# Performance work log

Hardware: AMD Instinct MI355X
Metric: run time of the kernel (lower is better)

The kernel has to match this reference:

```python
import jax, jax.numpy as jnp
import numpy as np

K = 75        # kpoints
L = 8         # number of labels (output_dim)


def _knn_nonconformity(q, t, train_label, k=K, num_labels=L):
    """Brute-force kNN (Euclidean) + distance-weighted nonconformity.
    q: [B, D] queries; t: [N, D] train bank; train_label: [N] int.
    Returns [B, num_labels]: for each class i, sum of 1/dist over the k
    nearest neighbors whose label != i (0 weight for zero distance)."""
    # squared distances [B, N]
    d2 = (jnp.sum(q * q, axis=1, keepdims=True)
          - 2.0 * q @ t.T
          + jnp.sum(t * t, axis=1)[None, :])
    d2 = jnp.maximum(d2, 0.0)
    neg_top, idx = jax.lax.top_k(-d2, k)          # k smallest d2
    dist = jnp.sqrt(jnp.maximum(-neg_top, 0.0))    # [B, k]
    safe = jnp.where(dist > 0, dist, 1.0)
    w = jnp.where(dist > 0, 1.0 / safe, 0.0)       # [B, k]
    mismatch = 1.0 - jax.nn.one_hot(train_label[idx], num_labels, dtype=w.dtype)  # [B,k,L]
    return jnp.einsum('bk,bkl->bl', w, mismatch)


def setup_inputs() -> dict:
    key = jax.random.key(0)
    ks = jax.random.split(key, 12)
    B, N, D, H, C = 1024, 50000, 83, 128, 10000
    s = lambda fan_in: 1.0 / np.sqrt(fan_in)
    return {
        'x': jax.random.normal(ks[0], (B, D), jnp.float32),
        'train_x': jax.random.normal(ks[1], (N, D), jnp.float32),
        'train_label': jax.random.randint(ks[2], (N,), 0, L, jnp.int32),
        'cali': jax.random.uniform(ks[3], (C,), jnp.float32) * 50.0,
        'W1': jax.random.normal(ks[4], (D, H), jnp.float32) * s(D),
        'b1': jnp.zeros((H,), jnp.float32),
        'W2': jax.random.normal(ks[5], (H, H), jnp.float32) * s(H),
        'b2': jnp.zeros((H,), jnp.float32),
        'W3': jax.random.normal(ks[6], (H, H), jnp.float32) * s(H),
        'b3': jnp.zeros((H,), jnp.float32),
        'W4': jax.random.normal(ks[7], (H, L), jnp.float32) * s(H),
        'b4': jnp.zeros((L,), jnp.float32),
    }


def reference(x, train_x, train_label, cali, W1, b1, W2, b2, W3, b3, W4, b4):
    relu = jax.nn.relu
    # query-side MLP (inference: dropout inactive)
    h1 = relu(x @ W1 + b1)
    h2 = relu(h1 @ W2 + b2)
    h3 = relu(h2 @ W3 + b3)
    out = jax.nn.softmax(h3 @ W4 + b4, axis=-1)
    # train-side feature banks (what each kNTree was fit on)
    t1 = relu(train_x @ W1 + b1)
    t2 = relu(t1 @ W2 + b2)
    t3 = relu(t2 @ W3 + b3)
    t4 = jax.nn.softmax(t3 @ W4 + b4, axis=-1)
    # per-layer nonconformity [B, L], summed across the 5 layers
    total = (_knn_nonconformity(x, train_x, train_label)
             + _knn_nonconformity(h1, t1, train_label)
             + _knn_nonconformity(h2, t2, train_label)
             + _knn_nonconformity(h3, t3, train_label)
             + _knn_nonconformity(out, t4, train_label))
    # empirical p-value: fraction of calibration scores >= total nonconformity
    counts = jnp.sum(cali[None, None, :] >= total[:, :, None], axis=-1)  # [B, L]
    return counts.astype(jnp.float32) / cali.shape[0]
```

## Files before the change

kernel.cpp:

```cpp
#include <hip/hip_runtime.h>
#include <math.h>

#define KNN 75
#define NL 8
#define NB 1024
#define NT 50000
#define NT_PAD 50048
#define NCALI 10000
#define KC 32
#define TT 128
#define NTB 391
#define SLOTS 16
#define CAP 6144
#define NSUB 2048
#define NSB 16
#define SSTRIDE 24
#define SOFF 11
#define RSEL 32
#define MLP8_BQ 1563
#define MLPB (2*NTB+16)
#define ARENA 34816

#define PB_Q    384
#define PB_BANK 18750
#define PB_W1   48
#define PB_W23  64
#define PREP_BLOCKS (PB_Q+PB_BANK+PB_W1+2*PB_W23)

typedef __attribute__((ext_vector_type(8))) short bf16x8;
typedef __attribute__((ext_vector_type(4))) float f32x4;

__device__ __forceinline__ int swz(int c){ return c + ((c>>5)<<2); }

__device__ __forceinline__ unsigned short f2bf_rn(float x){
  unsigned u = __float_as_uint(x);
  unsigned r = (u + 0x7FFFu + ((u>>16)&1u)) >> 16;
  return (unsigned short)r;
}
__device__ __forceinline__ float bf2f(unsigned short h){
  return __uint_as_float(((unsigned)h)<<16);
}
__device__ __forceinline__ bf16x8 ld8(const unsigned short* p){
  return *(const bf16x8*)p;
}
__device__ __forceinline__ void gl_lds16(const unsigned short* g, unsigned short* l){
  __builtin_amdgcn_global_load_lds(
      (const __attribute__((address_space(1))) void*)g,
      (__attribute__((address_space(3))) void*)l, 16, 0, 0);
}

__device__ __forceinline__ void pad_one(const float* __restrict__ in,
                                        float* __restrict__ out, int M,
                                        int Din, int Dout, int idx){
  if (idx >= M*Dout) return;
  int r = idx / Dout, c = idx - r*Dout;
  out[idx] = (c < Din) ? in[r*Din + c] : 0.f;
}
__device__ __forceinline__ void wsplit_one(const float* __restrict__ W, int kreal,
                                           int dp, unsigned short* __restrict__ WtH,
                                           unsigned short* __restrict__ WtL, int idx){
  int n = idx / dp, k = idx - n*dp;
  float v = (k < kreal) ? W[(size_t)k*128 + n] : 0.f;
  unsigned short h = f2bf_rn(v);
  WtH[idx] = h;
  WtL[idx] = f2bf_rn(v - bf2f(h));
}
__global__ void prep_k(const float* __restrict__ x, float* __restrict__ xq0,
                       const float* __restrict__ txr, float* __restrict__ tbA,
                       const float* __restrict__ W1, unsigned short* wt1H, unsigned short* wt1L,
                       const float* __restrict__ W2, unsigned short* wt2H, unsigned short* wt2L,
                       const float* __restrict__ W3, unsigned short* wt3H, unsigned short* wt3L){
  int b = blockIdx.x, tid = threadIdx.x;
  if (b < PB_Q){
    pad_one(x, xq0, NB, 83, 96, b*256 + tid);
  } else if (b < PB_Q + PB_BANK){
    pad_one(txr, tbA, NT, 83, 96, (b-PB_Q)*256 + tid);
  } else if (b < PB_Q + PB_BANK + PB_W1){
    wsplit_one(W1, 83, 96,  wt1H, wt1L, (b-PB_Q-PB_BANK)*256 + tid);
  } else if (b < PB_Q + PB_BANK + PB_W1 + PB_W23){
    wsplit_one(W2, 128, 128, wt2H, wt2L, (b-PB_Q-PB_BANK-PB_W1)*256 + tid);
  } else {
    wsplit_one(W3, 128, 128, wt3H, wt3L, (b-PB_Q-PB_BANK-PB_W1-PB_W23)*256 + tid);
  }
}

__global__ void conv_norm_k(
    const float* __restrict__ XA, unsigned short* __restrict__ HA,
    unsigned short* __restrict__ LA, float* __restrict__ nA, int MA,
    const float* __restrict__ XB, unsigned short* __restrict__ HB,
    unsigned short* __restrict__ LB, float* __restrict__ nB, int MB,
    int dp)
{
  int w = threadIdx.x>>6, lane = threadIdx.x&63;
  int row = blockIdx.x*4 + w;
  const float* src; unsigned short* dh; unsigned short* dl; float* nrm;
  if (row < MA){
    src=&XA[(size_t)row*dp]; dh=&HA[(size_t)row*dp]; dl=&LA[(size_t)row*dp]; nrm=&nA[row];
  } else {
    int r2 = row - MA;
    if (r2 >= MB) return;
    src=&XB[(size_t)r2*dp]; dh=&HB[(size_t)r2*dp]; dl=&LB[(size_t)r2*dp]; nrm=&nB[r2];
  }
  float s=0.f;
  for (int c=lane*2; c<dp; c+=128){
    float2 v = *(const float2*)&src[c];
    s += v.x*v.x + v.y*v.y;
    unsigned short h0 = f2bf_rn(v.x), h1 = f2bf_rn(v.y);
    float r0 = v.x - bf2f(h0), r1 = v.y - bf2f(h1);
    ushort2 hh; hh.x=h0; hh.y=h1;
    ushort2 ll; ll.x=f2bf_rn(r0); ll.y=f2bf_rn(r1);
    *(ushort2*)&dh[c]=hh;
    *(ushort2*)&dl[c]=ll;
  }
  #pragma unroll
  for (int off=32;off>0;off>>=1) s += __shfl_down(s, off, 64);
  if (lane==0) *nrm=s;
}

__device__ __forceinline__ void find_bin(int* hist, int* part, int nb, int Krem,
                                         int tid, int* s_B, int* s_lob){
  int ch = nb>>8;
  int base = tid*ch;
  int s=0;
  for (int b=base;b<base+ch;b++) s+=hist[b];
  int lane = tid & 63, wv = tid>>6;
  int v = s;
  #pragma unroll
  for (int off=1; off<64; off<<=1){
    int u = __shfl_up(v, off, 64);
    if (lane >= off) v += u;
  }
  if (lane==63) part[wv] = v;
  __syncthreads();
  int wbase = 0;
  #pragma unroll
  for (int w2=0; w2<4; w2++) wbase += (w2 < wv) ? part[w2] : 0;
  v += wbase;
  int excl = v - s;
  if (v >= Krem && excl < Krem){
    int lob = excl, B = base + ch - 1;
    for (int b=base;b<base+ch;b++){
      if (lob + hist[b] >= Krem){ B=b; break; }
      lob += hist[b];
    }
    *s_B = B; *s_lob = lob;
  }
  if (tid==255 && v < Krem){ *s_B = nb-1; *s_lob = 0; }
  __syncthreads();
}

__global__ __launch_bounds__(256) void sel64_k(const unsigned* __restrict__ skeys,
                                               unsigned* __restrict__ Tthr){
  __shared__ unsigned buf[NSUB];
  __shared__ int hist[2048];
  __shared__ int part[256];
  __shared__ int sB, sLob;
  int tid=threadIdx.x, q=blockIdx.x;
  for (int i=tid;i<NSUB;i+=256) buf[i]=skeys[(size_t)q*NSUB+i];
  int Krem=RSEL;
  for (int i=tid;i<2048;i+=256) hist[i]=0;
  __syncthreads();
  for (int i=tid;i<NSUB;i+=256) atomicAdd(&hist[buf[i]>>21],1);
  __syncthreads();
  find_bin(hist,part,2048,Krem,tid,&sB,&sLob);
  unsigned pre=(unsigned)sB; Krem-=sLob;
  for (int i=tid;i<2048;i+=256) hist[i]=0;
  __syncthreads();
  for (int i=tid;i<NSUB;i+=256){ unsigned k=buf[i]; if ((k>>21)==pre) atomicAdd(&hist[(k>>10)&0x7FFu],1); }
  __syncthreads();
  find_bin(hist,part,2048,Krem,tid,&sB,&sLob);
  pre=(pre<<11)|(unsigned)sB; Krem-=sLob;
  for (int i=tid;i<1024;i+=256) hist[i]=0;
  __syncthreads();
  for (int i=tid;i<NSUB;i+=256){ unsigned k=buf[i]; if ((k>>10)==pre) atomicAdd(&hist[k&0x3FFu],1); }
  __syncthreads();
  find_bin(hist,part,1024,Krem,tid,&sB,&sLob);
  if (tid==0) Tthr[q]=(pre<<10)|(unsigned)sB;
}

#define MFMA_SEC(BHC, BLC, AH, AL)                                               \
  _Pragma("unroll")                                                              \
  for (int tj=0;tj<8;tj++){                                                      \
    int rowB = tj*16 + col;                                                      \
    int sw = (((quad + (rowB>>1)) & 3) << 3);                                    \
    bf16x8 bh = *(const bf16x8*)&(BHC)[rowB*32 + sw];                            \
    bf16x8 bl = *(const bf16x8*)&(BLC)[rowB*32 + sw];                            \
    acc[tj] = __builtin_amdgcn_mfma_f32_16x16x32_bf16(AH, bh, acc[tj], 0,0,0);   \
    acc[tj] = __builtin_amdgcn_mfma_f32_16x16x32_bf16(AH, bl, acc[tj], 0,0,0);   \
    acc[tj] = __builtin_amdgcn_mfma_f32_16x16x32_bf16(AL, bh, acc[tj], 0,0,0);   \
  }

#define MFMA_KLOOP(ROWMAP)                                                       \
  size_t aoff = (size_t)(qbase + w*16 + col)*dp + quad*8;                        \
  const unsigned short* pAH = QH + aoff;                                         \
  const unsigned short* pAL = QL + aoff;                                         \
  int i0 = tid,      row0 = i0>>2, sg0 = ((i0&3) - (row0>>1)) & 3;               \
  int i1 = tid+256,  row1 = i1>>2, sg1 = ((i1&3) - (row1>>1)) & 3;               \
  size_t g0 = (size_t)(ROWMAP(n0+row0))*dp + (size_t)sg0*8;                      \
  size_t g1 = (size_t)(ROWMAP(n0+row1))*dp + (size_t)sg1*8;                      \
  f32x4 acc[8];                                                                  \
  _Pragma("unroll")                                                              \
  for (int tj=0;tj<8;tj++){ f32x4 z={0.f,0.f,0.f,0.f}; acc[tj]=z; }              \
  gl_lds16(TH + g0, BH0 + i0*8);                                                 \
  gl_lds16(TH + g1, BH0 + i1*8);                                                 \
  gl_lds16(TL + g0, BL0 + i0*8);                                                 \
  gl_lds16(TL + g1, BL0 + i1*8);                                                 \
  bf16x8 xh = ld8(pAH), xl = ld8(pAL);                                           \
  bf16x8 yh = xh, yl = xl;                                                       \
  _Pragma("unroll")                                                              \
  for (int kc=0; kc<kchunks; kc+=2){                                             \
    __syncthreads();                                                             \
    if (kc+1 < kchunks){                                                         \
      size_t ko=(size_t)(kc+1)*32;                                               \
      gl_lds16(TH + g0 + ko, BH1 + i0*8);                                        \
      gl_lds16(TH + g1 + ko, BH1 + i1*8);                                        \
      gl_lds16(TL + g0 + ko, BL1 + i0*8);                                        \
      gl_lds16(TL + g1 + ko, BL1 + i1*8);                                        \
      yh = ld8(pAH + ko); yl = ld8(pAL + ko);                                    \
    }                                                                            \
    MFMA_SEC(BH0, BL0, xh, xl);                                                  \
    if (kc+1 < kchunks){                                                         \
      __syncthreads();                                                           \
      if (kc+2 < kchunks){                                                       \
        size_t ko=(size_t)(kc+2)*32;                                             \
        gl_lds16(TH + g0 + ko, BH0 + i0*8);                                      \
        gl_lds16(TH + g1 + ko, BH0 + i1*8);                                      \
        gl_lds16(TL + g0 + ko, BL0 + i0*8);                                      \
        gl_lds16(TL + g1 + ko, BL0 + i1*8);                                      \
        xh = ld8(pAH + ko); xl = ld8(pAL + ko);                                  \
      }                                                                          \
      MFMA_SEC(BH1, BL1, yh, yl);                                                \
    }                                                                            \
  }

#define ROW_ID(r) (r)
#define ROW_SUB(r) ((r)*SSTRIDE + SOFF)

template<int KCH>
__global__ __launch_bounds__(256) void dist_mfma_k(
    const unsigned short* __restrict__ QH, const unsigned short* __restrict__ QL,
    const unsigned short* __restrict__ TH, const unsigned short* __restrict__ TL,
    const float* __restrict__ qn, const float* __restrict__ tn,
    const int* __restrict__ labels, const unsigned* __restrict__ Tthr,
    unsigned* __restrict__ slab)
{
  constexpr int dp = KCH*32;
  __shared__ __align__(16) unsigned short smem[4*4096];
  unsigned short* BH0 = smem;
  unsigned short* BH1 = smem + 4096;
  unsigned short* BL0 = smem + 8192;
  unsigned short* BL1 = smem + 12288;
  unsigned (*hitbuf)[SLOTS] = (unsigned (*)[SLOTS])smem;
  int* hcnt = (int*)(smem + 4096);
  int b = blockIdx.x;
  int xcd = b & 7, s = b >> 3;
  int qb = s & 15, tslot = s >> 4;
  int t_blk = xcd + 8*tslot;
  if (t_blk >= NTB) return;
  int tid = threadIdx.x, w = tid>>6, lane = tid&63;
  int quad = lane>>4, col = lane&15;
  int qbase = qb*64;
  int n0 = t_blk*TT;
  constexpr int kchunks = KCH;

  MFMA_KLOOP(ROW_ID)

  __syncthreads();
  if (tid<64) hcnt[tid]=0;
  __syncthreads();
  float qnr[4]; unsigned Tq[4]; float thrF[4];
  #pragma unroll
  for (int r=0;r<4;r++){
    int q = qbase + w*16 + quad*4 + r;
    qnr[r]  = qn[q];
    Tq[r]   = Tthr[q];
    thrF[r] = __uint_as_float(Tq[r] | 7u);
  }
  #pragma unroll
  for (int tj=0;tj<8;tj++){
    int t = n0 + tj*16 + col;
    if (t < NT){
      float tnv = tn[t];
      unsigned lab = (unsigned)labels[t];
      #pragma unroll
      for (int r=0;r<4;r++){
        float d2 = fmaf(-2.f, acc[tj][r], qnr[r] + tnv);
        if (d2 <= thrF[r]){
          float d2c = fmaxf(d2, 0.f);
          unsigned key = (__float_as_uint(d2c)&0xFFFFFFF8u) | lab;
          if (key < Tq[r]){
            int ql = w*16 + quad*4 + r;
            int idx = atomicAdd(&hcnt[ql], 1);
            if (idx < SLOTS-1) hitbuf[ql][1+idx] = key;
          }
        }
      }
    }
  }
  __syncthreads();
  if (tid<64) hitbuf[tid][0]=(unsigned)hcnt[tid];
  __syncthreads();
  {
    int q = tid>>2, sub = (tid&3)*4;
    uint4 v = *(uint4*)&hitbuf[q][sub];
    *(uint4*)&slab[((size_t)(qbase+q)*NTB + t_blk)*SLOTS + sub] = v;
  }
}

template<int KCH>
__device__ __forceinline__ void distsub_body(char* smc, int b,
    const unsigned short* __restrict__ QH, const unsigned short* __restrict__ QL,
    const unsigned short* __restrict__ TH, const unsigned short* __restrict__ TL,
    const float* __restrict__ qn, const float* __restrict__ tn,
    const int* __restrict__ labels, unsigned* __restrict__ keys)
{
  constexpr int dp = KCH*32;
  unsigned short* BH0 = (unsigned short*)smc;
  unsigned short* BH1 = BH0 + 4096;
  unsigned short* BL0 = BH0 + 8192;
  unsigned short* BL1 = BH0 + 12288;
  int qb = b & 15, t_blk = b >> 4;
  int tid = threadIdx.x, w = tid>>6, lane = tid&63;
  int quad = lane>>4, col = lane&15;
  int qbase = qb*64;
  int n0 = t_blk*TT;
  constexpr int kchunks = KCH;

  MFMA_KLOOP(ROW_SUB)

  float qnr[4];
  #pragma unroll
  for (int r=0;r<4;r++)
    qnr[r] = qn[qbase + w*16 + quad*4 + r];
  #pragma unroll
  for (int tj=0;tj<8;tj++){
    int sI = n0 + tj*16 + col;
    int g  = sI*SSTRIDE + SOFF;
    float tnv = tn[g];
    unsigned lab = (unsigned)labels[g];
    #pragma unroll
    for (int r=0;r<4;r++){
      float d2 = fmaxf(fmaf(-2.f, acc[tj][r], qnr[r] + tnv), 0.f);
      unsigned key = (__float_as_uint(d2)&0xFFFFFFF8u) | lab;
      int q = qbase + w*16 + quad*4 + r;
      keys[(size_t)q*NSUB + sI] = key;
    }
  }
}

template<int KCH>
__device__ __forceinline__ void mlp_body(char* smc, int b,
    const unsigned short* __restrict__ bkH, const unsigned short* __restrict__ bkL,
    const unsigned short* __restrict__ qh,  const unsigned short* __restrict__ ql,
    const unsigned short* __restrict__ TH, const unsigned short* __restrict__ TL,
    const float* __restrict__ bias,
    float* __restrict__ OutB, unsigned short* __restrict__ SBH,
    unsigned short* __restrict__ SBL, float* __restrict__ nrmB,
    float* __restrict__ OutQ, unsigned short* __restrict__ SQH,
    unsigned short* __restrict__ SQL, float* __restrict__ nrmQ)
{
  constexpr int dp = KCH*32;
  unsigned short* BH0 = (unsigned short*)smc;
  unsigned short* BH1 = BH0 + 4096;
  unsigned short* BL0 = BH0 + 8192;
  unsigned short* BL1 = BH0 + 12288;
  bool isq = (b >= 2*NTB);
  const unsigned short* QH = isq ? qh : bkH;
  const unsigned short* QL = isq ? ql : bkL;
  float* Out = isq ? OutQ : OutB;
  unsigned short* SH = isq ? SQH : SBH;
  unsigned short* SL = isq ? SQL : SBL;
  float* nrm = isq ? nrmQ : nrmB;
  int M = isq ? NB : NT;
  int tid = threadIdx.x, w = tid>>6, lane = tid&63;
  int quad = lane>>4, col = lane&15;
  int qbase = (isq ? (b - 2*NTB) : b) * 64;
  int n0 = 0;
  constexpr int kchunks = KCH;

  MFMA_KLOOP(ROW_ID)

  float bb[8];
  #pragma unroll
  for (int tj=0;tj<8;tj++) bb[tj] = bias[tj*16 + col];
  #pragma unroll
  for (int r=0;r<4;r++){
    int row = qbase + w*16 + quad*4 + r;
    if (row < M){
      float vv[8]; float s=0.f;
      #pragma unroll
      for (int tj=0;tj<8;tj++){
        float v = acc[tj][r] + bb[tj];
        v = v > 0.f ? v : 0.f;
        vv[tj] = v;
        s += v*v;
        Out[(size_t)row*128 + tj*16 + col] = v;
      }
      #pragma unroll
      for (int off=1; off<16; off<<=1) s += __shfl_xor(s, off, 16);
      if (col==0) nrm[row] = s;
      #pragma unroll
      for (int tj=0;tj<8;tj++){
        unsigned short h = f2bf_rn(vv[tj]);
        SH[(size_t)row*128 + tj*16 + col] = h;
        SL[(size_t)row*128 + tj*16 + col] = f2bf_rn(vv[tj] - bf2f(h));
      }
    }
  }
}

template<int KCH>
__global__ __launch_bounds__(256) void mlp_mfma_k(
    const unsigned short* bkH, const unsigned short* bkL,
    const unsigned short* qh,  const unsigned short* ql,
    const unsigned short* TH, const unsigned short* TL,
    const float* bias,
    float* OutB, unsigned short* SBH, unsigned short* SBL, float* nrmB,
    float* OutQ, unsigned short* SQH, unsigned short* SQL, float* nrmQ)
{
  __shared__ __align__(16) char smc[32768];
  mlp_body<KCH>(smc, blockIdx.x, bkH,bkL,qh,ql,TH,TL,bias,
                OutB,SBH,SBL,nrmB,OutQ,SQH,SQL,nrmQ);
}

__device__ __forceinline__ void mlp8_body(char* smc, int b,
    const float* __restrict__ AB, const float* __restrict__ AQ,
    const float* __restrict__ W4, const float* __restrict__ b4,
    float* __restrict__ OutB, unsigned short* __restrict__ SBH,
    unsigned short* __restrict__ SBL, float* __restrict__ nrmB,
    float* __restrict__ OutQ, unsigned short* __restrict__ SQH,
    unsigned short* __restrict__ SQL, float* __restrict__ nrmQ)
{
  float* Ws = (float*)smc;
  int tid = threadIdx.x;
  for (int i=tid;i<1024;i+=256) Ws[i]=W4[i];
  __syncthreads();
  bool isq = (b >= MLP8_BQ);
  int r = (isq ? (b-MLP8_BQ) : b)*32 + (tid>>3), c = tid&7;
  int M = isq ? NB : NT;
  if (r >= M) return;
  const float* A = isq ? AQ : AB;
  float* Out = isq ? OutQ : OutB;
  unsigned short* SH = isq ? SQH : SBH;
  unsigned short* SL = isq ? SQL : SBL;
  float* nrm = isq ? nrmQ : nrmB;
  const float* a = &A[(size_t)r*128];
  float acc = b4[c];
  #pragma unroll 16
  for (int k=0;k<128;k++) acc += a[k]*Ws[k*8+c];
  int lane = tid & 63, base = lane & ~7;
  float v[8];
  #pragma unroll
  for (int j=0;j<8;j++) v[j] = __shfl(acc, base+j, 64);
  float m=-1e30f;
  #pragma unroll
  for (int j=0;j<8;j++) m = v[j]>m ? v[j] : m;
  float s=0.f;
  #pragma unroll
  for (int j=0;j<8;j++){ v[j]=__expf(v[j]-m); s+=v[j]; }
  float inv=1.f/s;
  float nn=0.f;
  #pragma unroll
  for (int j=0;j<8;j++){ float pv=v[j]*inv; v[j]=pv; nn+=pv*pv; }
  float* p = &Out[(size_t)r*32];
  float pv = v[c];
  p[c]    = pv;
  p[8+c]  = 0.f;
  p[16+c] = 0.f;
  p[24+c] = 0.f;
  unsigned short h = f2bf_rn(pv);
  SH[(size_t)r*32 + c]    = h;
  SL[(size_t)r*32 + c]    = f2bf_rn(pv - bf2f(h));
  SH[(size_t)r*32 + 8+c]  = 0; SL[(size_t)r*32 + 8+c]  = 0;
  SH[(size_t)r*32 + 16+c] = 0; SL[(size_t)r*32 + 16+c] = 0;
  SH[(size_t)r*32 + 24+c] = 0; SL[(size_t)r*32 + 24+c] = 0;
  if (c==0) nrm[r] = nn;
}

__device__ void final_body(char* sm, int q,
    const unsigned* __restrict__ slab,
    const float* __restrict__ Qm, const float* __restrict__ Tm,
    const float* __restrict__ qn, const float* __restrict__ tn,
    const int* __restrict__ labels,
    float* __restrict__ tot, int first, int dp)
{
  int* hist = (int*)sm;
  int* part = (int*)(sm+8192);
  unsigned* buf = (unsigned*)(sm+9216);
  unsigned* lowbuf = (unsigned*)(sm+33792);
  float* qrow = (float*)(sm+34176);
  int* s_i = (int*)(sm+34688);
  float* s_w = (float*)(sm+34708);
  int tid=threadIdx.x;
  if (tid==0){ for (int j=0;j<9;j++) s_w[j]=0.f; s_i[2]=0; s_i[3]=0; s_i[4]=0; }
  __syncthreads();

  const unsigned* sq = slab + (size_t)q*NTB*SLOTS;
  for (int sidx=tid; sidx<NTB; sidx+=256){
    const unsigned* s = sq + (size_t)sidx*SLOTS;
    uint4 a = *(const uint4*)s;
    unsigned cnt = a.x;
    if (cnt > SLOTS-1){ s_i[4]=1; continue; }
    if (!cnt) continue;
    int base = atomicAdd(&s_i[2], (int)cnt);
    if (base + (int)cnt <= CAP){
      buf[base] = a.y;
      if (cnt>=2) buf[base+1] = a.z;
      if (cnt>=3) buf[base+2] = a.w;
      for (unsigned w=4; w<=cnt; w++) buf[base+w-1] = s[w];
    }
  }
  __syncthreads();
  int total = s_i[2];
  int bad = s_i[4];

#define CONTRIB(kk) do{ float d2_=__uint_as_float((kk)&0xFFFFFFF8u); \
    if (d2_>0.f){ float w_=1.0f/sqrtf(d2_); \
      atomicAdd(&s_w[8],w_); atomicAdd(&s_w[(kk)&7u],w_); } }while(0)

  unsigned T; int Krem=KNN;
  if (!bad && total>=KNN && total<=CAP){
    for (int i=tid;i<2048;i+=256) hist[i]=0;
    __syncthreads();
    for (int i=tid;i<total;i+=256) atomicAdd(&hist[buf[i]>>21],1);
    __syncthreads();
    find_bin(hist,part,2048,Krem,tid,&s_i[0],&s_i[1]);
    unsigned pre=(unsigned)s_i[0]; Krem-=s_i[1];
    for (int i=tid;i<2048;i+=256) hist[i]=0;
    __syncthreads();
    for (int i=tid;i<total;i+=256){ unsigned k=buf[i]; if ((k>>21)==pre) atomicAdd(&hist[(k>>10)&0x7FFu],1); }
    __syncthreads();
    find_bin(hist,part,2048,Krem,tid,&s_i[0],&s_i[1]);
    pre=(pre<<11)|(unsigned)s_i[0]; Krem-=s_i[1];
    for (int i=tid;i<1024;i+=256) hist[i]=0;
    __syncthreads();
    for (int i=tid;i<total;i+=256){ unsigned k=buf[i]; if ((k>>10)==pre) atomicAdd(&hist[k&0x3FFu],1); }
    __syncthreads();
    find_bin(hist,part,1024,Krem,tid,&s_i[0],&s_i[1]);
    T=(pre<<10)|(unsigned)s_i[0]; Krem-=s_i[1];
    __syncthreads();
    for (int i=tid;i<total;i+=256){ unsigned k=buf[i]; if (k<T) CONTRIB(k); }
  } else {
    if (tid==0) s_i[2]=0;
    for (int i=tid;i<dp;i+=256) qrow[i]=Qm[(size_t)q*dp+i];
    __syncthreads();
    float qq=qn[q];
    auto KEY=[&](int t)->unsigned{
      const float* br=&Tm[(size_t)t*dp];
      float dot=0.f;
      for (int k2=0;k2<dp;k2++) dot+=qrow[k2]*br[k2];
      float d2=fmaxf(qq-2.f*dot+tn[t],0.f);
      return (__float_as_uint(d2)&0xFFFFFFF8u)|(unsigned)labels[t];
    };
    for (int i=tid;i<2048;i+=256) hist[i]=0;
    __syncthreads();
    for (int t=tid;t<NT;t+=256) atomicAdd(&hist[KEY(t)>>21],1);
    __syncthreads();
    find_bin(hist,part,2048,Krem,tid,&s_i[0],&s_i[1]);
    int c=hist[s_i[0]]; Krem-=s_i[1];
    unsigned prefix=(unsigned)s_i[0]; int shift=21;
    if (c > CAP){
      __syncthreads();
      for (int i=tid;i<2048;i+=256) hist[i]=0;
      __syncthreads();
      for (int t=tid;t<NT;t+=256){ unsigned k=KEY(t); if ((k>>21)==prefix) atomicAdd(&hist[(k>>10)&0x7FFu],1); }
      __syncthreads();
      find_bin(hist,part,2048,Krem,tid,&s_i[0],&s_i[1]);
      c=hist[s_i[0]]; Krem-=s_i[1]; prefix=(prefix<<11)|(unsigned)s_i[0]; shift=10;
    }
    if (c > CAP){
      __syncthreads();
      for (int i=tid;i<1024;i+=256) hist[i]=0;
      __syncthreads();
      for (int t=tid;t<NT;t+=256){ unsigned k=KEY(t); if ((k>>10)==prefix) atomicAdd(&hist[k&0x3FFu],1); }
      __syncthreads();
      find_bin(hist,part,1024,Krem,tid,&s_i[0],&s_i[1]);
      c=hist[s_i[0]]; Krem-=s_i[1]; prefix=(prefix<<10)|(unsigned)s_i[0]; shift=0;
    }
    if (c <= CAP){
      for (int t=tid;t<NT;t+=256){
        unsigned k=KEY(t); unsigned pp=k>>shift;
        if (pp==prefix){ int j=atomicAdd(&s_i[2],1); if (j<CAP) buf[j]=k; }
        else if (pp<prefix){ int j=atomicAdd(&s_i[3],1); if (j<96) lowbuf[j]=k; }
      }
      __syncthreads();
      int sh=shift;
      while (sh>0){
        int nsh=(sh==21)?10:0;
        int nb=1<<(sh-nsh);
        __syncthreads();
        for (int i=tid;i<nb;i+=256) hist[i]=0;
        __syncthreads();
        int cc=s_i[2];
        for (int i=tid;i<cc;i+=256) atomicAdd(&hist[(buf[i]>>nsh)&(unsigned)(nb-1)],1);
        __syncthreads();
        find_bin(hist,part,nb,Krem,tid,&s_i[0],&s_i[1]);
        Krem-=s_i[1]; prefix=(prefix<<(sh-nsh))|(unsigned)s_i[0]; sh=nsh;
      }
      T=prefix;
      __syncthreads();
      int lowc=s_i[3], cc=s_i[2];
      for (int i=tid;i<lowc;i+=256){ unsigned k=lowbuf[i]; CONTRIB(k); }
      for (int i=tid;i<cc;i+=256){ unsigned k=buf[i]; if (k<T) CONTRIB(k); }
    } else {
      T=prefix;
      for (int t=tid;t<NT;t+=256){ unsigned k=KEY(t); if (k<T) CONTRIB(k); }
    }
  }
  __syncthreads();
  if (tid==0){
    float d2=__uint_as_float(T&0xFFFFFFF8u);
    float w=(d2>0.f)?(1.0f/sqrtf(d2)):0.f;
    s_w[8] += (float)Krem*w;
    s_w[T&7u] += (float)Krem*w;
  }
  __syncthreads();
  if (tid<8){
    float contrib = s_w[8]-s_w[tid];
    size_t o=(size_t)q*NL+tid;
    tot[o] = first ? contrib : tot[o]+contrib;
  }
#undef CONTRIB
}

__global__ __launch_bounds__(256) void final_k(
    const unsigned* slab, const float* Qm, const float* Tm,
    const float* qn, const float* tn, const int* labels,
    float* tot, int first, int dp)
{
  __shared__ __align__(16) char sm[ARENA];
  final_body(sm, blockIdx.x, slab, Qm, Tm, qn, tn, labels, tot, first, dp);
}

template<int KSUB, int KMLP, int M8>
__global__ __launch_bounds__(256) void fused_k(
    int nf,
    const unsigned* slab, const float* Qm, const float* Tm,
    const float* qnF, const float* tnF, float* tot, int first, int dpF,
    const unsigned short* qhS, const unsigned short* qlS,
    const unsigned short* bkHS, const unsigned short* bkLS,
    const float* qnS, const float* tnS, unsigned* skeys,
    const int* labels,
    const unsigned short* bkHM, const unsigned short* bkLM,
    const unsigned short* qhM, const unsigned short* qlM,
    const unsigned short* wtH, const unsigned short* wtL, const float* bias,
    float* OutB, unsigned short* SBH, unsigned short* SBL, float* nrmB,
    float* OutQ, unsigned short* SQH, unsigned short* SQL, float* nrmQ,
    const float* AB8, const float* AQ8, const float* W4, const float* b4)
{
  __shared__ __align__(16) char sm[ARENA];
  int b = blockIdx.x;
  if (b < nf){
    final_body(sm, b, slab, Qm, Tm, qnF, tnF, labels, tot, first, dpF);
    return;
  }
  b -= nf;
  if (b < 16*NSB){
    distsub_body<KSUB>(sm, b, qhS, qlS, bkHS, bkLS, qnS, tnS, labels, skeys);
    return;
  }
  b -= 16*NSB;
  if constexpr (KMLP > 0){
    mlp_body<KMLP>(sm, b, bkHM,bkLM,qhM,qlM, wtH,wtL, bias,
                   OutB,SBH,SBL,nrmB,OutQ,SQH,SQL,nrmQ);
  } else if constexpr (M8){
    mlp8_body(sm, b, AB8, AQ8, W4, b4, OutB,SBH,SBL,nrmB,OutQ,SQH,SQL,nrmQ);
  }
}

__global__ void pvalue_k(const float* __restrict__ tot, const float* __restrict__ cali,
                         float* __restrict__ out){
  __shared__ float t8[NL];
  __shared__ int part[4][NL];
  int tid=threadIdx.x, q=blockIdx.x;
  if (tid<NL) t8[tid]=tot[(size_t)q*NL+tid];
  __syncthreads();
  float th[NL];
  #pragma unroll
  for (int c=0;c<NL;c++) th[c]=t8[c];
  int cnt[NL];
  #pragma unroll
  for (int c=0;c<NL;c++) cnt[c]=0;
  for (int i=tid;i<NCALI;i+=256){
    float v=cali[i];
    #pragma unroll
    for (int c=0;c<NL;c++) cnt[c] += (v>=th[c]) ? 1 : 0;
  }
  #pragma unroll
  for (int c=0;c<NL;c++){
    #pragma unroll
    for (int off=32;off>0;off>>=1) cnt[c]+=__shfl_down(cnt[c],off,64);
  }
  if ((tid&63)==0){
    #pragma unroll
    for (int c=0;c<NL;c++) part[tid>>6][c]=cnt[c];
  }
  __syncthreads();
  if (tid<NL){
    int s=part[0][tid]+part[1][tid]+part[2][tid]+part[3][tid];
    out[(size_t)q*NL+tid] = (float)s / 10000.f;
  }
}

extern "C" void kernel_launch(void* const* d_in, const int* in_sizes, int n_in,
                              void* d_out, int out_size, void* d_ws, size_t ws_size,
                              hipStream_t stream) {
  const float* x   = (const float*)d_in[0];
  const float* txr = (const float*)d_in[1];
  const int*   lbl = (const int*)  d_in[2];
  const float* cal = (const float*)d_in[3];
  const float* W1  = (const float*)d_in[4];
  const float* b1  = (const float*)d_in[5];
  const float* W2  = (const float*)d_in[6];
  const float* b2  = (const float*)d_in[7];
  const float* W3  = (const float*)d_in[8];
  const float* b3  = (const float*)d_in[9];
  const float* W4  = (const float*)d_in[10];
  const float* b4  = (const float*)d_in[11];
  float* out = (float*)d_out;
  float* ws  = (float*)d_ws;

  size_t off=0;
  float* xq0=ws+off; off+=(size_t)NB*96;
  float* xq1=ws+off; off+=(size_t)NB*128;
  float* xq2=ws+off; off+=(size_t)NB*128;
  float* xq3=ws+off; off+=(size_t)NB*128;
  float* xq4=ws+off; off+=(size_t)NB*32;
  float* tbA=ws+off; off+=(size_t)NT*128;
  float* tbB=ws+off; off+=(size_t)NT*128;
  float* tb4=ws+off; off+=(size_t)NT*32;
  float* qnb=ws+off; off+=(size_t)5*NB;
  float* tnb=ws+off; off+=(size_t)5*NT;
  float* tot=ws+off; off+=(size_t)NB*NL;
  unsigned* sT=(unsigned*)(ws+off); off+=NB;
  unsigned short* qH0=(unsigned short*)(ws+off); off+=(size_t)NB*48;
  unsigned short* qL0=(unsigned short*)(ws+off); off+=(size_t)NB*48;
  unsigned short* qH1=(unsigned short*)(ws+off); off+=(size_t)NB*64;
  unsigned short* qL1=(unsigned short*)(ws+off); off+=(size_t)NB*64;
  unsigned short* qH2=(unsigned short*)(ws+off); off+=(size_t)NB*64;
  unsigned short* qL2=(unsigned short*)(ws+off); off+=(size_t)NB*64;
  unsigned short* qH3=(unsigned short*)(ws+off); off+=(size_t)NB*64;
  unsigned short* qL3=(unsigned short*)(ws+off); off+=(size_t)NB*64;
  unsigned short* qH4=(unsigned short*)(ws+off); off+=(size_t)NB*16;
  unsigned short* qL4=(unsigned short*)(ws+off); off+=(size_t)NB*16;
  unsigned short* bkAH=(unsigned short*)(ws+off); off+=(size_t)NT_PAD*64;
  unsigned short* bkAL=(unsigned short*)(ws+off); off+=(size_t)NT_PAD*64;
  unsigned short* bkBH=(unsigned short*)(ws+off); off+=(size_t)NT_PAD*64;
  unsigned short* bkBL=(unsigned short*)(ws+off); off+=(size_t)NT_PAD*64;
  unsigned short* wt1H=(unsigned short*)(ws+off); off+=(size_t)128*48;
  unsigned short* wt1L=(unsigned short*)(ws+off); off+=(size_t)128*48;
  unsigned short* wt2H=(unsigned short*)(ws+off); off+=(size_t)128*64;
  unsigned short* wt2L=(unsigned short*)(ws+off); off+=(size_t)128*64;
  unsigned short* wt3H=(unsigned short*)(ws+off); off+=(size_t)128*64;
  unsigned short* wt3L=(unsigned short*)(ws+off); off+=(size_t)128*64;
  off=(off+3)&~(size_t)3;
  unsigned* slab=(unsigned*)(ws+off); off+=(size_t)NB*NTB*SLOTS;
  unsigned* skeys=(unsigned*)(ws+off); off+=(size_t)NB*NSUB;

  float* tnb0=tnb, *tnb1=tnb+NT, *tnb2=tnb+2*NT, *tnb3=tnb+3*NT, *tnb4=tnb+4*NT;

  prep_k<<<PREP_BLOCKS,256,0,stream>>>(x,xq0,txr,tbA,
                                       W1,wt1H,wt1L,W2,wt2H,wt2L,W3,wt3H,wt3L);
  conv_norm_k<<<(NT+NB)/4,256,0,stream>>>(tbA, bkAH, bkAL, tnb0, NT,
                                          xq0, qH0, qL0, qnb+0*NB, NB, 96);

  fused_k<3,3,0><<<16*NSB + MLPB,256,0,stream>>>(0,
      nullptr,nullptr,nullptr,nullptr,nullptr,nullptr,0,0,
      qH0,qL0, bkAH,bkAL, qnb+0*NB, tnb0, skeys, lbl,
      bkAH,bkAL, qH0,qL0, wt1H,wt1L, b1,
      tbB,bkBH,bkBL,tnb1, xq1,qH1,qL1,qnb+1*NB,
      nullptr,nullptr,nullptr,nullptr);
  sel64_k<<<NB,256,0,stream>>>(skeys,sT);
  dist_mfma_k<3><<<8*16*49,256,0,stream>>>(qH0,qL0,bkAH,bkAL,qnb+0*NB,tnb0,lbl,sT,slab);

  fused_k<4,0,0><<<NB + 16*NSB,256,0,stream>>>(NB,
      slab, xq0, tbA, qnb+0*NB, tnb0, tot, 1, 96,
      qH1,qL1, bkBH,bkBL, qnb+1*NB, tnb1, skeys, lbl,
      nullptr,nullptr,nullptr,nullptr,nullptr,nullptr,nullptr,
      nullptr,nullptr,nullptr,nullptr,nullptr,nullptr,nullptr,nullptr,
      nullptr,nullptr,nullptr,nullptr);
  mlp_mfma_k<4><<<MLPB,256,0,stream>>>(bkBH,bkBL, qH1,qL1, wt2H,wt2L, b2,
                                       tbA,bkAH,bkAL,tnb2, xq2,qH2,qL2,qnb+2*NB);
  sel64_k<<<NB,256,0,stream>>>(skeys,sT);
  dist_mfma_k<4><<<8*16*49,256,0,stream>>>(qH1,qL1,bkBH,bkBL,qnb+1*NB,tnb1,lbl,sT,slab);

  fused_k<4,0,0><<<NB + 16*NSB,256,0,stream>>>(NB,
      slab, xq1, tbB, qnb+1*NB, tnb1, tot, 0, 128,
      qH2,qL2, bkAH,bkAL, qnb+2*NB, tnb2, skeys, lbl,
      nullptr,nullptr,nullptr,nullptr,nullptr,nullptr,nullptr,
      nullptr,nullptr,nullptr,nullptr,nullptr,nullptr,nullptr,nullptr,
      nullptr,nullptr,nullptr,nullptr);
  mlp_mfma_k<4><<<MLPB,256,0,stream>>>(bkAH,bkAL, qH2,qL2, wt3H,wt3L, b3,
                                       tbB,bkBH,bkBL,tnb3, xq3,qH3,qL3,qnb+3*NB);
  sel64_k<<<NB,256,0,stream>>>(skeys,sT);
  dist_mfma_k<4><<<8*16*49,256,0,stream>>>(qH2,qL2,bkAH,bkAL,qnb+2*NB,tnb2,lbl,sT,slab);

  fused_k<4,0,1><<<NB + 16*NSB + MLP8_BQ+32,256,0,stream>>>(NB,
      slab, xq2, tbA, qnb+2*NB, tnb2, tot, 0, 128,
      qH3,qL3, bkBH,bkBL, qnb+3*NB, tnb3, skeys, lbl,
      nullptr,nullptr,nullptr,nullptr,nullptr,nullptr,nullptr,
      tb4,bkAH,bkAL,tnb4, xq4,qH4,qL4,qnb+4*NB,
      tbB, xq3, W4, b4);
  sel64_k<<<NB,256,0,stream>>>(skeys,sT);
  dist_mfma_k<4><<<8*16*49,256,0,stream>>>(qH3,qL3,bkBH,bkBL,qnb+3*NB,tnb3,lbl,sT,slab);

  fused_k<1,0,0><<<NB + 16*NSB,256,0,stream>>>(NB,
      slab, xq3, tbB, qnb+3*NB, tnb3, tot, 0, 128,
      qH4,qL4, bkAH,bkAL, qnb+4*NB, tnb4, skeys, lbl,
      nullptr,nullptr,nullptr,nullptr,nullptr,nullptr,nullptr,
      nullptr,nullptr,nullptr,nullptr,nullptr,nullptr,nullptr,nullptr,
      nullptr,nullptr,nullptr,nullptr);
  sel64_k<<<NB,256,0,stream>>>(skeys,sT);
  dist_mfma_k<1><<<8*16*49,256,0,stream>>>(qH4,qL4,bkAH,bkAL,qnb+4*NB,tnb4,lbl,sT,slab);

  final_k<<<NB,256,0,stream>>>(slab, xq4, tb4, qnb+4*NB, tnb4, lbl, tot, 0, 32);

  pvalue_k<<<NB,256,0,stream>>>(tot,cal,out);
}
```

Measured before the change: 646.3 us.

## Process four train tiles per block in distance kernel with register-held queries

Each dist_mfma_k block now walks four train tiles instead of one. The query A fragments are loaded once into registers and reused across all four, and staging of the next tile's bank data overlaps the current tile's MFMAs. The grid shrinks by about 4x, which cuts block launch and per-block setup overhead, and hitbuf/hcnt move to their own shared buffers. The cost is more registers per thread (aH/aL for every K chunk), more shared memory, and fewer blocks to hide latency.

```diff
diff --git a/kernel.cpp b/kernel.cpp
--- a/kernel.cpp
+++ b/kernel.cpp
@@ -20,6 +20,8 @@
 #define MLP8_BQ 1563
 #define MLPB (2*NTB+16)
 #define ARENA 34816
+#define TPB 4
+#define DMB (8*16*13)
 
 #define PB_Q    384
 #define PB_BANK 18750
@@ -228,13 +230,22 @@
         gl_lds16(TL + g0 + ko, BL0 + i0*8);                                      \
         gl_lds16(TL + g1 + ko, BL0 + i1*8);                                      \
         xh = ld8(pAH + ko); xl = ld8(pAL + ko);                                  \
-      }                                                                          \
+      }                                                                            \
       MFMA_SEC(BH1, BL1, yh, yl);                                                \
     }                                                                            \
   }
 
 #define ROW_ID(r) (r)
 #define ROW_SUB(r) ((r)*SSTRIDE + SOFF)
+
+#define STG(N0V, KO, DH, DL) do{                                                \
+    size_t _g0 = (size_t)((N0V) + row0)*dp + (size_t)sg0*8 + (KO);              \
+    size_t _g1 = (size_t)((N0V) + row1)*dp + (size_t)sg1*8 + (KO);              \
+    gl_lds16(TH + _g0, (DH) + i0*8);                                            \
+    gl_lds16(TH + _g1, (DH) + i1*8);                                            \
+    gl_lds16(TL + _g0, (DL) + i0*8);                                            \
+    gl_lds16(TL + _g1, (DL) + i1*8);                                            \
+  }while(0)
 
 template<int KCH>
 __global__ __launch_bounds__(256) void dist_mfma_k(
@@ -246,28 +257,37 @@
 {
   constexpr int dp = KCH*32;
   __shared__ __align__(16) unsigned short smem[4*4096];
+  __shared__ unsigned hitbuf[64][SLOTS];
+  __shared__ int hcnt[64];
   unsigned short* BH0 = smem;
   unsigned short* BH1 = smem + 4096;
   unsigned short* BL0 = smem + 8192;
   unsigned short* BL1 = smem + 12288;
-  unsigned (*hitbuf)[SLOTS] = (unsigned (*)[SLOTS])smem;
-  int* hcnt = (int*)(smem + 4096);
   int b = blockIdx.x;
   int xcd = b & 7, s = b >> 3;
-  int qb = s & 15, tslot = s >> 4;
-  int t_blk = xcd + 8*tslot;
-  if (t_blk >= NTB) return;
+  int qb = s & 15, jslot = s >> 4;
   int tid = threadIdx.x, w = tid>>6, lane = tid&63;
   int quad = lane>>4, col = lane&15;
   int qbase = qb*64;
-  int n0 = t_blk*TT;
-  constexpr int kchunks = KCH;
-
-  MFMA_KLOOP(ROW_ID)
-
-  __syncthreads();
-  if (tid<64) hcnt[tid]=0;
-  __syncthreads();
+
+  int n0s[TPB]; int TV=0;
+  #pragma unroll
+  for (int i=0;i<TPB;i++){
+    int lin = jslot*TPB + i;
+    int tb  = xcd + 8*lin;
+    n0s[i] = tb*TT;
+    if (lin < 49 && tb < NTB) TV = i+1;
+  }
+  if (TV == 0) return;
+
+  size_t aoff = (size_t)(qbase + w*16 + col)*dp + quad*8;
+  bf16x8 aH[KCH], aL[KCH];
+  #pragma unroll
+  for (int c=0;c<KCH;c++){ aH[c]=ld8(QH+aoff+c*32); aL[c]=ld8(QL+aoff+c*32); }
+
+  int i0 = tid,      row0 = i0>>2, sg0 = ((i0&3) - (row0>>1)) & 3;
+  int i1 = tid+256,  row1 = i1>>2, sg1 = ((i1&3) - (row1>>1)) & 3;
+
   float qnr[4]; unsigned Tq[4]; float thrF[4];
   #pragma unroll
   for (int r=0;r<4;r++){
@@ -276,36 +296,68 @@
     Tq[r]   = Tthr[q];
     thrF[r] = __uint_as_float(Tq[r] | 7u);
   }
-  #pragma unroll
-  for (int tj=0;tj<8;tj++){
-    int t = n0 + tj*16 + col;
-    if (t < NT){
-      float tnv = tn[t];
-      unsigned lab = (unsigned)labels[t];
-      #pragma unroll
-      for (int r=0;r<4;r++){
-        float d2 = fmaf(-2.f, acc[tj][r], qnr[r] + tnv);
-        if (d2 <= thrF[r]){
-          float d2c = fmaxf(d2, 0.f);
-          unsigned key = (__float_as_uint(d2c)&0xFFFFFFF8u) | lab;
-          if (key < Tq[r]){
-            int ql = w*16 + quad*4 + r;
-            int idx = atomicAdd(&hcnt[ql], 1);
-            if (idx < SLOTS-1) hitbuf[ql][1+idx] = key;
+
+  f32x4 acc[8];
+  #pragma unroll
+  for (int tj=0;tj<8;tj++){ f32x4 z={0.f,0.f,0.f,0.f}; acc[tj]=z; }
+
+  STG(n0s[0], 0, BH0, BL0);
+  int buf = 0;
+
+  #pragma unroll
+  for (int ti=0; ti<TPB; ti++){
+    if (ti >= TV) break;
+    int n0 = n0s[ti];
+    #pragma unroll
+    for (int c=0;c<KCH;c++){
+      __syncthreads();
+      if (c+1 < KCH){
+        if (buf==0) STG(n0, (size_t)(c+1)*32, BH1, BL1);
+        else        STG(n0, (size_t)(c+1)*32, BH0, BL0);
+      } else if (ti+1 < TV){
+        if (buf==0) STG(n0s[ti+1], 0, BH1, BL1);
+        else        STG(n0s[ti+1], 0, BH0, BL0);
+      }
+      if (c==0 && tid<64) hcnt[tid]=0;
+      if (buf==0){ MFMA_SEC(BH0, BL0, aH[c], aL[c]); }
+      else       { MFMA_SEC(BH1, BL1, aH[c], aL[c]); }
+      buf ^= 1;
+    }
+    __syncthreads();
+    #pragma unroll
+    for (int tj=0;tj<8;tj++){
+      int t = n0 + tj*16 + col;
+      if (t < NT){
+        float tnv = tn[t];
+        unsigned lab = (unsigned)labels[t];
+        #pragma unroll
+        for (int r=0;r<4;r++){
+          float d2 = fmaf(-2.f, acc[tj][r], qnr[r] + tnv);
+          if (d2 <= thrF[r]){
+            float d2c = fmaxf(d2, 0.f);
+            unsigned key = (__float_as_uint(d2c)&0xFFFFFFF8u) | lab;
+            if (key < Tq[r]){
+              int ql = w*16 + quad*4 + r;
+              int idx = atomicAdd(&hcnt[ql], 1);
+              if (idx < SLOTS-1) hitbuf[ql][1+idx] = key;
+            }
           }
         }
       }
     }
-  }
-  __syncthreads();
-  if (tid<64) hitbuf[tid][0]=(unsigned)hcnt[tid];
-  __syncthreads();
-  {
-    int q = tid>>2, sub = (tid&3)*4;
-    uint4 v = *(uint4*)&hitbuf[q][sub];
-    *(uint4*)&slab[((size_t)(qbase+q)*NTB + t_blk)*SLOTS + sub] = v;
-  }
-}
+    __syncthreads();
+    if (tid<64) hitbuf[tid][0]=(unsigned)hcnt[tid];
+    __syncthreads();
+    {
+      int q = tid>>2, sub = (tid&3)*4;
+      uint4 v = *(uint4*)&hitbuf[q][sub];
+      *(uint4*)&slab[((size_t)(qbase+q)*NTB + (n0>>7))*SLOTS + sub] = v;
+    }
+    #pragma unroll
+    for (int tj=0;tj<8;tj++){ f32x4 z={0.f,0.f,0.f,0.f}; acc[tj]=z; }
+  }
+}
+#undef STG
 
 template<int KCH>
 __device__ __forceinline__ void distsub_body(char* smc, int b,
@@ -771,7 +823,7 @@
       tbB,bkBH,bkBL,tnb1, xq1,qH1,qL1,qnb+1*NB,
       nullptr,nullptr,nullptr,nullptr);
   sel64_k<<<NB,256,0,stream>>>(skeys,sT);
-  dist_mfma_k<3><<<8*16*49,256,0,stream>>>(qH0,qL0,bkAH,bkAL,qnb+0*NB,tnb0,lbl,sT,slab);
+  dist_mfma_k<3><<<DMB,256,0,stream>>>(qH0,qL0,bkAH,bkAL,qnb+0*NB,tnb0,lbl,sT,slab);
 
   fused_k<4,0,0><<<NB + 16*NSB,256,0,stream>>>(NB,
       slab, xq0, tbA, qnb+0*NB, tnb0, tot, 1, 96,
@@ -782,7 +834,7 @@
   mlp_mfma_k<4><<<MLPB,256,0,stream>>>(bkBH,bkBL, qH1,qL1, wt2H,wt2L, b2,
                                        tbA,bkAH,bkAL,tnb2, xq2,qH2,qL2,qnb+2*NB);
   sel64_k<<<NB,256,0,stream>>>(skeys,sT);
-  dist_mfma_k<4><<<8*16*49,256,0,stream>>>(qH1,qL1,bkBH,bkBL,qnb+1*NB,tnb1,lbl,sT,slab);
+  dist_mfma_k<4><<<DMB,256,0,stream>>>(qH1,qL1,bkBH,bkBL,qnb+1*NB,tnb1,lbl,sT,slab);
 
   fused_k<4,0,0><<<NB + 16*NSB,256,0,stream>>>(NB,
       slab, xq1, tbB, qnb+1*NB, tnb1, tot, 0, 128,
@@ -793,7 +845,7 @@
   mlp_mfma_k<4><<<MLPB,256,0,stream>>>(bkAH,bkAL, qH2,qL2, wt3H,wt3L, b3,
                                        tbB,bkBH,bkBL,tnb3, xq3,qH3,qL3,qnb+3*NB);
   sel64_k<<<NB,256,0,stream>>>(skeys,sT);
-  dist_mfma_k<4><<<8*16*49,256,0,stream>>>(qH2,qL2,bkAH,bkAL,qnb+2*NB,tnb2,lbl,sT,slab);
+  dist_mfma_k<4><<<DMB,256,0,stream>>>(qH2,qL2,bkAH,bkAL,qnb+2*NB,tnb2,lbl,sT,slab);
 
   fused_k<4,0,1><<<NB + 16*NSB + MLP8_BQ+32,256,0,stream>>>(NB,
       slab, xq2, tbA, qnb+2*NB, tnb2, tot, 0, 128,
@@ -802,7 +854,7 @@
       tb4,bkAH,bkAL,tnb4, xq4,qH4,qL4,qnb+4*NB,
       tbB, xq3, W4, b4);
   sel64_k<<<NB,256,0,stream>>>(skeys,sT);
-  dist_mfma_k<4><<<8*16*49,256,0,stream>>>(qH3,qL3,bkBH,bkBL,qnb+3*NB,tnb3,lbl,sT,slab);
+  dist_mfma_k<4><<<DMB,256,0,stream>>>(qH3,qL3,bkBH,bkBL,qnb+3*NB,tnb3,lbl,sT,slab);
 
   fused_k<1,0,0><<<NB + 16*NSB,256,0,stream>>>(NB,
       slab, xq3, tbB, qnb+3*NB, tnb3, tot, 0, 128,
@@ -811,7 +863,7 @@
       nullptr,nullptr,nullptr,nullptr,nullptr,nullptr,nullptr,nullptr,
       nullptr,nullptr,nullptr,nullptr);
   sel64_k<<<NB,256,0,stream>>>(skeys,sT);
-  dist_mfma_k<1><<<8*16*49,256,0,stream>>>(qH4,qL4,bkAH,bkAL,qnb+4*NB,tnb4,lbl,sT,slab);
+  dist_mfma_k<1><<<DMB,256,0,stream>>>(qH4,qL4,bkAH,bkAL,qnb+4*NB,tnb4,lbl,sT,slab);
 
   final_k<<<NB,256,0,stream>>>(slab, xq4, tb4, qnb+4*NB, tnb4, lbl, tot, 0, 32);
 
```

Result: slower. 782.6 us (+21.1%).
